# Kernel tuning notes

Measured on AMD Instinct MI355X. Metric: run time of the kernel, lower is better.

## Reference

```python
import jax, jax.numpy as jnp
import numpy as np

N = 100_000
E = 1_600_000
IN_DIM = 21
HID = 256
OUT = 256


def setup_inputs() -> dict:
    key = jax.random.key(0)
    ks = jax.random.split(key, 10)
    node_scalar = jax.random.normal(ks[0], (N, IN_DIM), dtype=jnp.float32)
    edge_index = jax.random.randint(ks[1], (2, E), 0, N, dtype=jnp.int64)
    s_in = 1.0 / np.sqrt(IN_DIM)
    s_h = 1.0 / np.sqrt(HID)
    W_in = jax.random.uniform(ks[2], (IN_DIM, HID), jnp.float32, -s_in, s_in)
    b_in = jax.random.uniform(ks[3], (HID,), jnp.float32, -s_in, s_in)
    W_self = jax.random.uniform(ks[4], (HID, HID), jnp.float32, -s_h, s_h)
    b_self = jax.random.uniform(ks[5], (HID,), jnp.float32, -s_h, s_h)
    W_nei = jax.random.uniform(ks[6], (HID, HID), jnp.float32, -s_h, s_h)
    b_nei = jax.random.uniform(ks[7], (HID,), jnp.float32, -s_h, s_h)
    W_out = jax.random.uniform(ks[8], (HID, OUT), jnp.float32, -s_h, s_h)
    b_out = jax.random.uniform(ks[9], (OUT,), jnp.float32, -s_h, s_h)
    return {
        "node_scalar": node_scalar,
        "W_in": W_in, "b_in": b_in,
        "W_self": W_self, "b_self": b_self,
        "W_nei": W_nei, "b_nei": b_nei,
        "W_out": W_out, "b_out": b_out,
        "edge_index": edge_index,
    }


def reference(node_scalar, W_in, b_in, W_self, b_self, W_nei, b_nei, W_out, b_out, edge_index):
    # x = relu(Linear(node_scalar)); dropout is identity in eval mode
    x = jax.nn.relu(node_scalar @ W_in + b_in)           # (N, H)
    n = x.shape[0]
    src, dst = edge_index[0], edge_index[1]
    msg = x[src]                                          # (E, H) gather
    agg = jax.ops.segment_sum(msg, dst, num_segments=n)   # (N, H) scatter-add
    deg = jax.ops.segment_sum(jnp.ones((dst.shape[0],), dtype=x.dtype), dst, num_segments=n)
    agg = agg / jnp.maximum(deg, 1.0)[:, None]            # degree mean (clamp_min 1)
    h = jax.nn.relu(x @ W_self + b_self + agg @ W_nei + b_nei)
    g = h.mean(axis=0)                                    # global mean pool -> (H,)
    return g @ W_out + b_out                              # (OUT,)
```

## Files before the change

### kernel.cpp

```cpp
#include <hip/hip_runtime.h>
#include <hip/hip_bf16.h>

#define HID 256
#define IND 21
#define PB 6400
#define MAXB 512

typedef short short8 __attribute__((ext_vector_type(8)));
typedef float floatx16 __attribute__((ext_vector_type(16)));
typedef float floatx2 __attribute__((ext_vector_type(2)));

__device__ inline unsigned short f2bf(float f) {
  __hip_bfloat16 h = __float2bfloat16(f);
  union { __hip_bfloat16 h; unsigned short u; } c;
  c.h = h;
  return c.u;
}

__device__ inline unsigned int pk_bf16_trunc(floatx2 p) {
  union { float f; unsigned int u; } a, b;
  a.f = p.x; b.f = p.y;
  return (b.u & 0xffff0000u) | (a.u >> 16);
}

__device__ inline void acc8p(uint2 v, floatx2* a) {
  a[0] += __builtin_amdgcn_cvt_pk_f32_fp8((int)v.x, false);
  a[1] += __builtin_amdgcn_cvt_pk_f32_fp8((int)v.x, true);
  a[2] += __builtin_amdgcn_cvt_pk_f32_fp8((int)v.y, false);
  a[3] += __builtin_amdgcn_cvt_pk_f32_fp8((int)v.y, true);
}

__device__ inline short8 mk_s8(unsigned a, unsigned b, unsigned c, unsigned d) {
  union { uint4 u; short8 s; } x; x.u = make_uint4(a, b, c, d); return x.s;
}

__device__ inline short8 dec8(uint2 v) {
  unsigned w0 = pk_bf16_trunc(__builtin_amdgcn_cvt_pk_f32_fp8((int)v.x, false));
  unsigned w1 = pk_bf16_trunc(__builtin_amdgcn_cvt_pk_f32_fp8((int)v.x, true));
  unsigned w2 = pk_bf16_trunc(__builtin_amdgcn_cvt_pk_f32_fp8((int)v.y, false));
  unsigned w3 = pk_bf16_trunc(__builtin_amdgcn_cvt_pk_f32_fp8((int)v.y, true));
  return mk_s8(w0, w1, w2, w3);
}

__device__ inline void gl16(const unsigned char* g, unsigned char* l) {
  __builtin_amdgcn_global_load_lds(
      (const __attribute__((address_space(1))) unsigned char*)g,
      (__attribute__((address_space(3))) unsigned char*)l, 16, 0, 0);
}

__global__ __launch_bounds__(256) void k_front(
    const float* __restrict__ ns, const float* __restrict__ Win,
    const float* __restrict__ bin, uint2* __restrict__ xq2,
    uint2* __restrict__ Aqx,
    const float* __restrict__ Wself, const float* __restrict__ Wnei,
    unsigned short* __restrict__ Bf16,
    const int* __restrict__ dst, int* __restrict__ bcnt,
    int N, int E, int nb2, int G1) {
  int blk = blockIdx.x;
  int tid = threadIdx.x;
  if (blk < G1) {
    __shared__ float s[8][IND];
    __shared__ float fx[8][257];
    int nb = blk * 8;
    if (tid < 8 * IND) {
      int idx = nb * IND + tid;
      s[tid / IND][tid % IND] = (idx < N * IND) ? ns[idx] : 0.f;
    }
    float w[IND];
#pragma unroll
    for (int k = 0; k < IND; k++) w[k] = Win[k * HID + tid];
    float b = bin[tid];
    __syncthreads();
#pragma unroll
    for (int j = 0; j < 8; j++) {
      float acc = b;
#pragma unroll
      for (int k = 0; k < IND; k++) acc += s[j][k] * w[k];
      fx[j][tid] = acc > 0.f ? acc : 0.f;
    }
    __syncthreads();
    {
      int j = tid & 7, u = tid >> 3;
      int node = nb + j;
      if (node < N) {
        const float* fp = &fx[j][u * 8];
        int lo0 = __builtin_amdgcn_cvt_pk_fp8_f32(fp[0], fp[1], 0, false);
        int w0  = __builtin_amdgcn_cvt_pk_fp8_f32(fp[2], fp[3], lo0, true);
        int lo1 = __builtin_amdgcn_cvt_pk_fp8_f32(fp[4], fp[5], 0, false);
        int w1  = __builtin_amdgcn_cvt_pk_fp8_f32(fp[6], fp[7], lo1, true);
        uint2 val = make_uint2((unsigned)w0, (unsigned)w1);
        xq2[(size_t)node * 32 + u] = val;
        int g = node >> 5, row = node & 31, c = u >> 1, hi = u & 1;
        Aqx[(size_t)(g * 16 + c) * 64 + hi * 32 + row] = val;
      }
    }
  } else if (blk < G1 + 256) {
    int n = blk - G1;
    int ct = n >> 5, l5 = n & 31;
#pragma unroll
    for (int t = 0; t < 2; t++) {
      int k = tid + t * 256;
      float v = (k < HID) ? Wself[k * HID + n] : Wnei[(k - HID) * HID + n];
      int c = k >> 4, kin = k & 15;
      int lane = (kin >> 3) * 32 + l5;
      int j = kin & 7;
      Bf16[(size_t)((c * 8 + ct) * 64 + lane) * 8 + j] = f2bf(v);
    }
  } else {
    __shared__ int lh[MAXB];
    int e0 = (blk - G1 - 256) * PB;
    for (int b = tid; b < nb2; b += 256) lh[b] = 0;
    __syncthreads();
    int c = min(PB, E - e0);
    for (int i = tid; i < c; i += 256) atomicAdd(&lh[dst[e0 + i] >> 8], 1);
    __syncthreads();
    for (int b = tid; b < nb2; b += 256)
      if (lh[b]) atomicAdd(&bcnt[b], lh[b]);
  }
}

__global__ __launch_bounds__(512) void k_bscan(
    const int* __restrict__ bcnt, int* __restrict__ bbase, int* __restrict__ bcur,
    int* __restrict__ row_start, int E, int N, int nb2) {
  __shared__ int ts[512];
  int tid = threadIdx.x;
  int v = (tid < nb2) ? bcnt[tid] : 0;
  ts[tid] = v;
  __syncthreads();
  for (int off = 1; off < 512; off <<= 1) {
    int t = (tid >= off) ? ts[tid - off] : 0;
    __syncthreads();
    ts[tid] += t;
    __syncthreads();
  }
  if (tid < nb2) { bbase[tid] = ts[tid] - v; bcur[tid] = ts[tid] - v; }
  if (tid == 0) { bbase[nb2] = E; row_start[N] = E; }
}

__global__ __launch_bounds__(256) void k_part(
    const int* __restrict__ src, const int* __restrict__ dst,
    int* __restrict__ bcur, unsigned int* __restrict__ ebuf, int E, int nb2) {
  __shared__ int lh[MAXB];
  int tid = threadIdx.x;
  int e0 = blockIdx.x * PB;
  for (int b = tid; b < nb2; b += 256) lh[b] = 0;
  __syncthreads();
  int cnt = min(PB, E - e0);
  for (int i = tid; i < cnt; i += 256) atomicAdd(&lh[dst[e0 + i] >> 8], 1);
  __syncthreads();
  for (int b = tid; b < nb2; b += 256) {
    int c = lh[b];
    lh[b] = (c > 0) ? atomicAdd(&bcur[b], c) : 0;
  }
  __syncthreads();
  for (int i = tid; i < cnt; i += 256) {
    int s = src[e0 + i];
    int d = dst[e0 + i];
    int pos = atomicAdd(&lh[d >> 8], 1);
    ebuf[pos] = ((unsigned)s << 8) | ((unsigned)d & 255u);
  }
}

__global__ __launch_bounds__(256) void k_fill2(
    const unsigned int* __restrict__ ebuf, const int* __restrict__ bbase,
    int* __restrict__ row_start, unsigned int* __restrict__ csr, int N) {
  __shared__ int lcnt[256];
  __shared__ int lcur[256];
  __shared__ int ts[256];
  int b = blockIdx.x;
  int tid = threadIdx.x;
  int start = bbase[b], end = bbase[b + 1];
  lcnt[tid] = 0;
  __syncthreads();
  for (int i = start + tid; i < end; i += 256)
    atomicAdd(&lcnt[ebuf[i] & 255u], 1);
  __syncthreads();
  int v = lcnt[tid];
  ts[tid] = v;
  __syncthreads();
  for (int off = 1; off < 256; off <<= 1) {
    int t = (tid >= off) ? ts[tid - off] : 0;
    __syncthreads();
    ts[tid] += t;
    __syncthreads();
  }
  int excl = start + ts[tid] - v;
  int node = (b << 8) + tid;
  if (node < N) row_start[node] = excl;
  lcur[tid] = excl;
  __syncthreads();
  for (int i = start + tid; i < end; i += 256) {
    unsigned int e = ebuf[i];
    int pos = atomicAdd(&lcur[e & 255u], 1);
    csr[pos] = e & ~255u;
  }
}

__global__ __launch_bounds__(256) void k_agg(
    const unsigned char* __restrict__ xqb, const unsigned int* __restrict__ csrb,
    const int* __restrict__ row_start, uint2* __restrict__ Aqagg, int N) {
  __shared__ uint2 ld[8][33];
  int tid = threadIdx.x;
  int lane = tid & 63;
  int w = tid >> 6;
  int half = lane >> 5;
  int l32 = lane & 31;
  unsigned lo = (unsigned)(l32 * 8);

  int nl = w * 2 + half;
  int wid = blockIdx.x * 8 + nl;
  int cw = (wid < N) ? wid : (N - 1);
  int start = row_start[cw];
  int end = row_start[cw + 1];
  int c = end - start;
  floatx2 a[4], b[4], d[4], e[4];
#pragma unroll
  for (int j = 0; j < 4; j++) {
    a[j] = (floatx2){0.f, 0.f}; b[j] = (floatx2){0.f, 0.f};
    d[j] = (floatx2){0.f, 0.f}; e[j] = (floatx2){0.f, 0.f};
  }

  int i = 0;
  while (i < c) {
    int nb = min(32, c - i);
    int sel = (l32 < nb) ? l32 : 0;
    unsigned idx = csrb[start + i + sel];
    int j = 0;
    for (; j + 8 <= nb; j += 8) {
      unsigned o0 = (unsigned)__shfl((int)idx, j + 0, 32) + lo;
      unsigned o1 = (unsigned)__shfl((int)idx, j + 1, 32) + lo;
      unsigned o2 = (unsigned)__shfl((int)idx, j + 2, 32) + lo;
      unsigned o3 = (unsigned)__shfl((int)idx, j + 3, 32) + lo;
      unsigned o4 = (unsigned)__shfl((int)idx, j + 4, 32) + lo;
      unsigned o5 = (unsigned)__shfl((int)idx, j + 5, 32) + lo;
      unsigned o6 = (unsigned)__shfl((int)idx, j + 6, 32) + lo;
      unsigned o7 = (unsigned)__shfl((int)idx, j + 7, 32) + lo;
      uint2 v0 = *(const uint2*)(xqb + o0);
      uint2 v1 = *(const uint2*)(xqb + o1);
      uint2 v2 = *(const uint2*)(xqb + o2);
      uint2 v3 = *(const uint2*)(xqb + o3);
      uint2 v4 = *(const uint2*)(xqb + o4);
      uint2 v5 = *(const uint2*)(xqb + o5);
      uint2 v6 = *(const uint2*)(xqb + o6);
      uint2 v7 = *(const uint2*)(xqb + o7);
      acc8p(v0, a); acc8p(v1, b); acc8p(v2, d); acc8p(v3, e);
      acc8p(v4, a); acc8p(v5, b); acc8p(v6, d); acc8p(v7, e);
    }
    for (; j + 4 <= nb; j += 4) {
      unsigned o0 = (unsigned)__shfl((int)idx, j + 0, 32) + lo;
      unsigned o1 = (unsigned)__shfl((int)idx, j + 1, 32) + lo;
      unsigned o2 = (unsigned)__shfl((int)idx, j + 2, 32) + lo;
      unsigned o3 = (unsigned)__shfl((int)idx, j + 3, 32) + lo;
      uint2 v0 = *(const uint2*)(xqb + o0);
      uint2 v1 = *(const uint2*)(xqb + o1);
      uint2 v2 = *(const uint2*)(xqb + o2);
      uint2 v3 = *(const uint2*)(xqb + o3);
      acc8p(v0, a); acc8p(v1, b); acc8p(v2, d); acc8p(v3, e);
    }
    for (; j < nb; j++) {
      unsigned o0 = (unsigned)__shfl((int)idx, j, 32) + lo;
      uint2 v0 = *(const uint2*)(xqb + o0);
      acc8p(v0, a);
    }
    i += nb;
  }
#pragma unroll
  for (int j = 0; j < 4; j++) a[j] += b[j] + d[j] + e[j];

  float inv = 1.0f / fmaxf((float)c, 1.0f);
  float f[8];
#pragma unroll
  for (int j = 0; j < 4; j++) {
    f[2 * j] = a[j].x * inv;
    f[2 * j + 1] = a[j].y * inv;
  }
  int lo0 = __builtin_amdgcn_cvt_pk_fp8_f32(f[0], f[1], 0, false);
  int w0  = __builtin_amdgcn_cvt_pk_fp8_f32(f[2], f[3], lo0, true);
  int lo1 = __builtin_amdgcn_cvt_pk_fp8_f32(f[4], f[5], 0, false);
  int w1  = __builtin_amdgcn_cvt_pk_fp8_f32(f[6], f[7], lo1, true);
  ld[nl][l32] = make_uint2((unsigned)w0, (unsigned)w1);
  __syncthreads();

  int g = blockIdx.x >> 2;
  int r0 = (blockIdx.x & 3) * 8;
  int s = tid >> 3, j = tid & 7;
  Aqagg[(size_t)g * 1024 + (size_t)s * 32 + r0 + j] = ld[j][s];
}

__global__ __launch_bounds__(256, 3) void k_h(
    const unsigned char* __restrict__ Aqx, const unsigned char* __restrict__ Aqagg,
    const unsigned char* __restrict__ Bf8, const float* __restrict__ bself,
    const float* __restrict__ bnei, float* __restrict__ hpart, int N, int nfull) {
  __shared__ __align__(16) unsigned char As[2][8192];
  __shared__ __align__(16) unsigned char Bs[2][16384];
  __shared__ float colsum[128];
  int bid = blockIdx.x;
  int bx, by;
  if (bid < nfull) {
    bx = (bid >> 4) * 8 + (bid & 7);
    by = (bid >> 3) & 1;
  } else {
    int rem = bid - nfull;
    bx = (nfull >> 1) + (rem >> 1);
    by = rem & 1;
  }
  int tid = threadIdx.x;
  int lane = tid & 63;
  int w = tid >> 6;
  int wr = w >> 1, wc = w & 1;
  int l32 = lane & 31, half = lane >> 5;
  int rowBase = bx * 128;

  if (tid < 128) colsum[tid] = 0.f;

  floatx16 acc[2][2];
#pragma unroll
  for (int i = 0; i < 2; i++)
#pragma unroll
    for (int j = 0; j < 2; j++) acc[i][j] = (floatx16)(0.f);

  size_t a_grp = (size_t)(bx * 4 + w) * 16 * 512;
  int lb = lane * 16;

  {
    const unsigned char* asrc = Aqx + a_grp + lb;
    gl16(asrc, As[0] + w * 2048);
    gl16(asrc + 1024, As[0] + w * 2048 + 1024);
#pragma unroll
    for (int fi = 0; fi < 4; fi++) {
      int ctg = by * 4 + fi;
      gl16(Bf8 + (size_t)(w * 8 + ctg) * 1024 + lb, Bs[0] + (w * 4 + fi) * 1024);
    }
  }

  for (int ch = 0; ch < 8; ch++) {
    int buf = ch & 1;
    __syncthreads();
    if (ch < 7) {
      int cn = ch + 1;
      const unsigned char* Aq = (cn < 4) ? Aqx : Aqagg;
      const unsigned char* asrc = Aq + a_grp + (size_t)(cn & 3) * 2048 + lb;
      unsigned char* ad = As[buf ^ 1] + w * 2048;
      gl16(asrc, ad);
      gl16(asrc + 1024, ad + 1024);
#pragma unroll
      for (int fi = 0; fi < 4; fi++) {
        int cg = cn * 4 + w;
        int ctg = by * 4 + fi;
        gl16(Bf8 + (size_t)(cg * 8 + ctg) * 1024 + lb,
             Bs[buf ^ 1] + (w * 4 + fi) * 1024);
      }
    }
#pragma unroll
    for (int cl = 0; cl < 4; cl++) {
      short8 afr[2];
#pragma unroll
      for (int rt = 0; rt < 2; rt++) {
        uint2 av = *(const uint2*)&As[buf][(wr * 2 + rt) * 2048 + cl * 512 + lane * 8];
        afr[rt] = dec8(av);
      }
#pragma unroll
      for (int ctw = 0; ctw < 2; ctw++) {
        short8 bfr = *(const short8*)&Bs[buf][(cl * 4 + wc * 2 + ctw) * 1024 + lane * 16];
#pragma unroll
        for (int rt = 0; rt < 2; rt++)
          acc[rt][ctw] = __builtin_amdgcn_mfma_f32_32x32x16_bf16(
              afr[rt], bfr, acc[rt][ctw], 0, 0, 0);
      }
    }
  }

#pragma unroll
  for (int ctw = 0; ctw < 2; ctw++) {
    int lcol = (wc * 2 + ctw) * 32 + l32;
    int gcol = by * 128 + lcol;
    float bb = bself[gcol] + bnei[gcol];
    float psum = 0.f;
#pragma unroll
    for (int rt = 0; rt < 2; rt++) {
#pragma unroll
      for (int r = 0; r < 16; r++) {
        int rw = rowBase + wr * 64 + rt * 32 + (r & 3) + 8 * (r >> 2) + 4 * half;
        float v = acc[rt][ctw][r] + bb;
        v = v > 0.f ? v : 0.f;
        if (rw < N) psum += v;
      }
    }
    atomicAdd(&colsum[lcol], psum);
  }
  __syncthreads();
  if (tid < 128) hpart[(size_t)bx * 256 + by * 128 + tid] = colsum[tid];
}

__global__ __launch_bounds__(256) void k_red(
    const float* __restrict__ hpart, float* __restrict__ gsum, int nbx) {
  int c = threadIdx.x;
  float s = 0.f;
  for (int i = blockIdx.x; i < nbx; i += gridDim.x)
    s += hpart[(size_t)i * 256 + c];
  atomicAdd(&gsum[c], s);
}

__global__ __launch_bounds__(HID) void k_out(
    const float* __restrict__ gsum, const float* __restrict__ Wout,
    const float* __restrict__ bout, float* __restrict__ out, float invN) {
  __shared__ float g[HID];
  int c = threadIdx.x;
  g[c] = gsum[c] * invN;
  __syncthreads();
  float acc = bout[c];
#pragma unroll 8
  for (int k = 0; k < HID; k++) acc += g[k] * Wout[k * HID + c];
  out[c] = acc;
}

extern "C" void kernel_launch(void* const* d_in, const int* in_sizes, int n_in,
                              void* d_out, int out_size, void* d_ws, size_t ws_size,
                              hipStream_t stream) {
  const float* ns    = (const float*)d_in[0];
  const float* Win   = (const float*)d_in[1];
  const float* bin   = (const float*)d_in[2];
  const float* Wself = (const float*)d_in[3];
  const float* bself = (const float*)d_in[4];
  const float* Wnei  = (const float*)d_in[5];
  const float* bnei  = (const float*)d_in[6];
  const float* Wout  = (const float*)d_in[7];
  const float* bout  = (const float*)d_in[8];
  const int*   eidx  = (const int*)d_in[9];

  int N = in_sizes[0] / IND;
  int E = in_sizes[9] / 2;
  const int* src = eidx;
  const int* dst = eidx + E;
  int nb2 = (N + 255) >> 8;
  int nbx = (N + 127) / 128;
  size_t NGU = (size_t)nbx * 4 * 16 * 64;

  unsigned int* xq     = (unsigned int*)d_ws;
  uint2* Aqx           = (uint2*)(xq + (size_t)N * 64);
  uint2* Aqagg         = Aqx + NGU;
  unsigned short* Bf16 = (unsigned short*)(Aqagg + NGU);
  unsigned int* csr  = (unsigned int*)(Bf16 + 256 * 512);
  unsigned int* ebuf = csr + E;
  int* row_start = (int*)(ebuf + E);
  int* bcnt      = row_start + N + 1;
  int* bbase     = bcnt + MAXB;
  int* bcur      = bbase + MAXB + 1;
  float* gsum    = (float*)(bcur + MAXB);
  float* hpart   = gsum + HID;

  hipMemsetAsync(bcnt, 0, MAXB * sizeof(int), stream);
  hipMemsetAsync(gsum, 0, HID * sizeof(float), stream);

  int G1 = (N + 7) / 8;
  int pgrid = (E + PB - 1) / PB;
  k_front<<<G1 + 256 + pgrid, 256, 0, stream>>>(
      ns, Win, bin, (uint2*)xq, Aqx, Wself, Wnei, Bf16, dst, bcnt,
      N, E, nb2, G1);

  k_bscan<<<1, 512, 0, stream>>>(bcnt, bbase, bcur, row_start, E, N, nb2);
  k_part<<<pgrid, 256, 0, stream>>>(src, dst, bcur, ebuf, E, nb2);
  k_fill2<<<nb2, 256, 0, stream>>>(ebuf, bbase, row_start, csr, N);

  int agrid = (N + 7) / 8;
  k_agg<<<agrid, 256, 0, stream>>>((const unsigned char*)xq, csr, row_start,
                                   Aqagg, N);

  int nblocks = nbx * 2;
  int nfull = (nblocks / 16) * 16;
  k_h<<<nblocks, 256, 0, stream>>>((const unsigned char*)Aqx,
                                   (const unsigned char*)Aqagg,
                                   (const unsigned char*)Bf16,
                                   bself, bnei, hpart, N, nfull);

  k_red<<<64, 256, 0, stream>>>(hpart, gsum, nbx);
  k_out<<<1, HID, 0, stream>>>(gsum, Wout, bout, (float*)d_out, 1.0f / (float)N);
}
```

Before: 284.1 us.

## Fuse neighbor aggregation into the GEMM kernel and drop hpart reduction

```diff
diff --git a/kernel.cpp b/kernel.cpp
--- a/kernel.cpp
+++ b/kernel.cpp
@@ -196,122 +196,110 @@
   }
 }
 
-__global__ __launch_bounds__(256) void k_agg(
+__global__ __launch_bounds__(256, 3) void k_hagg(
     const unsigned char* __restrict__ xqb, const unsigned int* __restrict__ csrb,
-    const int* __restrict__ row_start, uint2* __restrict__ Aqagg, int N) {
-  __shared__ uint2 ld[8][33];
+    const int* __restrict__ row_start, const unsigned char* __restrict__ Aqx,
+    const unsigned short* __restrict__ Bf16, const float* __restrict__ bself,
+    const float* __restrict__ bnei, float* __restrict__ gsum, int N) {
+  __shared__ __align__(16) unsigned char As[2][4096];
+  __shared__ __align__(16) unsigned char AggL[16384];
+  __shared__ float colsum[256];
   int tid = threadIdx.x;
   int lane = tid & 63;
   int w = tid >> 6;
-  int half = lane >> 5;
-  int l32 = lane & 31;
-  unsigned lo = (unsigned)(l32 * 8);
-
-  int nl = w * 2 + half;
-  int wid = blockIdx.x * 8 + nl;
-  int cw = (wid < N) ? wid : (N - 1);
-  int start = row_start[cw];
-  int end = row_start[cw + 1];
-  int c = end - start;
-  floatx2 a[4], b[4], d[4], e[4];
-#pragma unroll
-  for (int j = 0; j < 4; j++) {
-    a[j] = (floatx2){0.f, 0.f}; b[j] = (floatx2){0.f, 0.f};
-    d[j] = (floatx2){0.f, 0.f}; e[j] = (floatx2){0.f, 0.f};
-  }
-
-  int i = 0;
-  while (i < c) {
-    int nb = min(32, c - i);
-    int sel = (l32 < nb) ? l32 : 0;
-    unsigned idx = csrb[start + i + sel];
-    int j = 0;
-    for (; j + 8 <= nb; j += 8) {
-      unsigned o0 = (unsigned)__shfl((int)idx, j + 0, 32) + lo;
-      unsigned o1 = (unsigned)__shfl((int)idx, j + 1, 32) + lo;
-      unsigned o2 = (unsigned)__shfl((int)idx, j + 2, 32) + lo;
-      unsigned o3 = (unsigned)__shfl((int)idx, j + 3, 32) + lo;
-      unsigned o4 = (unsigned)__shfl((int)idx, j + 4, 32) + lo;
-      unsigned o5 = (unsigned)__shfl((int)idx, j + 5, 32) + lo;
-      unsigned o6 = (unsigned)__shfl((int)idx, j + 6, 32) + lo;
-      unsigned o7 = (unsigned)__shfl((int)idx, j + 7, 32) + lo;
-      uint2 v0 = *(const uint2*)(xqb + o0);
-      uint2 v1 = *(const uint2*)(xqb + o1);
-      uint2 v2 = *(const uint2*)(xqb + o2);
-      uint2 v3 = *(const uint2*)(xqb + o3);
-      uint2 v4 = *(const uint2*)(xqb + o4);
-      uint2 v5 = *(const uint2*)(xqb + o5);
-      uint2 v6 = *(const uint2*)(xqb + o6);
-      uint2 v7 = *(const uint2*)(xqb + o7);
-      acc8p(v0, a); acc8p(v1, b); acc8p(v2, d); acc8p(v3, e);
-      acc8p(v4, a); acc8p(v5, b); acc8p(v6, d); acc8p(v7, e);
-    }
-    for (; j + 4 <= nb; j += 4) {
-      unsigned o0 = (unsigned)__shfl((int)idx, j + 0, 32) + lo;
-      unsigned o1 = (unsigned)__shfl((int)idx, j + 1, 32) + lo;
-      unsigned o2 = (unsigned)__shfl((int)idx, j + 2, 32) + lo;
-      unsigned o3 = (unsigned)__shfl((int)idx, j + 3, 32) + lo;
-      uint2 v0 = *(const uint2*)(xqb + o0);
-      uint2 v1 = *(const uint2*)(xqb + o1);
-      uint2 v2 = *(const uint2*)(xqb + o2);
-      uint2 v3 = *(const uint2*)(xqb + o3);
-      acc8p(v0, a); acc8p(v1, b); acc8p(v2, d); acc8p(v3, e);
-    }
-    for (; j < nb; j++) {
-      unsigned o0 = (unsigned)__shfl((int)idx, j, 32) + lo;
-      uint2 v0 = *(const uint2*)(xqb + o0);
-      acc8p(v0, a);
-    }
-    i += nb;
-  }
-#pragma unroll
-  for (int j = 0; j < 4; j++) a[j] += b[j] + d[j] + e[j];
-
-  float inv = 1.0f / fmaxf((float)c, 1.0f);
-  float f[8];
-#pragma unroll
-  for (int j = 0; j < 4; j++) {
-    f[2 * j] = a[j].x * inv;
-    f[2 * j + 1] = a[j].y * inv;
-  }
-  int lo0 = __builtin_amdgcn_cvt_pk_fp8_f32(f[0], f[1], 0, false);
-  int w0  = __builtin_amdgcn_cvt_pk_fp8_f32(f[2], f[3], lo0, true);
-  int lo1 = __builtin_amdgcn_cvt_pk_fp8_f32(f[4], f[5], 0, false);
-  int w1  = __builtin_amdgcn_cvt_pk_fp8_f32(f[6], f[7], lo1, true);
-  ld[nl][l32] = make_uint2((unsigned)w0, (unsigned)w1);
-  __syncthreads();
-
-  int g = blockIdx.x >> 2;
-  int r0 = (blockIdx.x & 3) * 8;
-  int s = tid >> 3, j = tid & 7;
-  Aqagg[(size_t)g * 1024 + (size_t)s * 32 + r0 + j] = ld[j][s];
-}
-
-__global__ __launch_bounds__(256, 3) void k_h(
-    const unsigned char* __restrict__ Aqx, const unsigned char* __restrict__ Aqagg,
-    const unsigned char* __restrict__ Bf8, const float* __restrict__ bself,
-    const float* __restrict__ bnei, float* __restrict__ hpart, int N, int nfull) {
-  __shared__ __align__(16) unsigned char As[2][8192];
-  __shared__ __align__(16) unsigned char Bs[2][16384];
-  __shared__ float colsum[128];
-  int bid = blockIdx.x;
-  int bx, by;
-  if (bid < nfull) {
-    bx = (bid >> 4) * 8 + (bid & 7);
-    by = (bid >> 3) & 1;
-  } else {
-    int rem = bid - nfull;
-    bx = (nfull >> 1) + (rem >> 1);
-    by = rem & 1;
-  }
-  int tid = threadIdx.x;
-  int lane = tid & 63;
-  int w = tid >> 6;
-  int wr = w >> 1, wc = w & 1;
+  int bx = blockIdx.x;
+  int rowBase = bx * 64;
   int l32 = lane & 31, half = lane >> 5;
-  int rowBase = bx * 128;
-
-  if (tid < 128) colsum[tid] = 0.f;
+
+  colsum[tid] = 0.f;
+
+  int gi = w >> 1, kb = w & 1;
+  {
+    const unsigned char* asrc =
+        Aqx + (size_t)(bx * 2 + gi) * 8192 + kb * 1024 + lane * 16;
+    gl16(asrc, As[0] + gi * 2048 + kb * 1024);
+  }
+
+  {
+    unsigned lo = (unsigned)(l32 * 8);
+    unsigned u = (unsigned)l32;
+    unsigned ubase = (u >> 3) * 512 + ((u & 7) >> 1) * 64 + (u & 1) * 32;
+    uint2* AggL2 = (uint2*)AggL;
+    for (int pass = 0; pass < 8; ++pass) {
+      int nd = pass * 8 + w * 2 + half;
+      int wid = rowBase + nd;
+      int cw = (wid < N) ? wid : (N - 1);
+      int start = row_start[cw];
+      int end = row_start[cw + 1];
+      int c = end - start;
+      floatx2 a[4], b[4];
+#pragma unroll
+      for (int j = 0; j < 4; j++) {
+        a[j] = (floatx2){0.f, 0.f};
+        b[j] = (floatx2){0.f, 0.f};
+      }
+      int i = 0;
+      while (i < c) {
+        int nb = min(32, c - i);
+        int sel = (l32 < nb) ? l32 : 0;
+        unsigned idx = csrb[start + i + sel];
+        int j = 0;
+        for (; j + 8 <= nb; j += 8) {
+          unsigned o0 = (unsigned)__shfl((int)idx, j + 0, 32) + lo;
+          unsigned o1 = (unsigned)__shfl((int)idx, j + 1, 32) + lo;
+          unsigned o2 = (unsigned)__shfl((int)idx, j + 2, 32) + lo;
+          unsigned o3 = (unsigned)__shfl((int)idx, j + 3, 32) + lo;
+          unsigned o4 = (unsigned)__shfl((int)idx, j + 4, 32) + lo;
+          unsigned o5 = (unsigned)__shfl((int)idx, j + 5, 32) + lo;
+          unsigned o6 = (unsigned)__shfl((int)idx, j + 6, 32) + lo;
+          unsigned o7 = (unsigned)__shfl((int)idx, j + 7, 32) + lo;
+          uint2 v0 = *(const uint2*)(xqb + o0);
+          uint2 v1 = *(const uint2*)(xqb + o1);
+          uint2 v2 = *(const uint2*)(xqb + o2);
+          uint2 v3 = *(const uint2*)(xqb + o3);
+          uint2 v4 = *(const uint2*)(xqb + o4);
+          uint2 v5 = *(const uint2*)(xqb + o5);
+          uint2 v6 = *(const uint2*)(xqb + o6);
+          uint2 v7 = *(const uint2*)(xqb + o7);
+          acc8p(v0, a); acc8p(v1, b); acc8p(v2, a); acc8p(v3, b);
+          acc8p(v4, a); acc8p(v5, b); acc8p(v6, a); acc8p(v7, b);
+        }
+        for (; j + 4 <= nb; j += 4) {
+          unsigned o0 = (unsigned)__shfl((int)idx, j + 0, 32) + lo;
+          unsigned o1 = (unsigned)__shfl((int)idx, j + 1, 32) + lo;
+          unsigned o2 = (unsigned)__shfl((int)idx, j + 2, 32) + lo;
+          unsigned o3 = (unsigned)__shfl((int)idx, j + 3, 32) + lo;
+          uint2 v0 = *(const uint2*)(xqb + o0);
+          uint2 v1 = *(const uint2*)(xqb + o1);
+          uint2 v2 = *(const uint2*)(xqb + o2);
+          uint2 v3 = *(const uint2*)(xqb + o3);
+          acc8p(v0, a); acc8p(v1, b); acc8p(v2, a); acc8p(v3, b);
+        }
+        for (; j < nb; j++) {
+          unsigned o0 = (unsigned)__shfl((int)idx, j, 32) + lo;
+          uint2 v0 = *(const uint2*)(xqb + o0);
+          acc8p(v0, a);
+        }
+        i += nb;
+      }
+#pragma unroll
+      for (int j = 0; j < 4; j++) a[j] += b[j];
+
+      float inv = 1.0f / fmaxf((float)c, 1.0f);
+      float f[8];
+#pragma unroll
+      for (int j = 0; j < 4; j++) {
+        f[2 * j] = a[j].x * inv;
+        f[2 * j + 1] = a[j].y * inv;
+      }
+      int lo0 = __builtin_amdgcn_cvt_pk_fp8_f32(f[0], f[1], 0, false);
+      int w0  = __builtin_amdgcn_cvt_pk_fp8_f32(f[2], f[3], lo0, true);
+      int lo1 = __builtin_amdgcn_cvt_pk_fp8_f32(f[4], f[5], 0, false);
+      int w1  = __builtin_amdgcn_cvt_pk_fp8_f32(f[6], f[7], lo1, true);
+      AggL2[ubase + (unsigned)((nd >> 5) * 256 + (nd & 31))] =
+          make_uint2((unsigned)w0, (unsigned)w1);
+    }
+  }
 
   floatx16 acc[2][2];
 #pragma unroll
@@ -319,86 +307,74 @@
 #pragma unroll
     for (int j = 0; j < 2; j++) acc[i][j] = (floatx16)(0.f);
 
-  size_t a_grp = (size_t)(bx * 4 + w) * 16 * 512;
-  int lb = lane * 16;
-
-  {
-    const unsigned char* asrc = Aqx + a_grp + lb;
-    gl16(asrc, As[0] + w * 2048);
-    gl16(asrc + 1024, As[0] + w * 2048 + 1024);
-#pragma unroll
-    for (int fi = 0; fi < 4; fi++) {
-      int ctg = by * 4 + fi;
-      gl16(Bf8 + (size_t)(w * 8 + ctg) * 1024 + lb, Bs[0] + (w * 4 + fi) * 1024);
-    }
-  }
-
-  for (int ch = 0; ch < 8; ch++) {
-    int buf = ch & 1;
-    __syncthreads();
-    if (ch < 7) {
-      int cn = ch + 1;
-      const unsigned char* Aq = (cn < 4) ? Aqx : Aqagg;
-      const unsigned char* asrc = Aq + a_grp + (size_t)(cn & 3) * 2048 + lb;
-      unsigned char* ad = As[buf ^ 1] + w * 2048;
-      gl16(asrc, ad);
-      gl16(asrc + 1024, ad + 1024);
-#pragma unroll
-      for (int fi = 0; fi < 4; fi++) {
-        int cg = cn * 4 + w;
-        int ctg = by * 4 + fi;
-        gl16(Bf8 + (size_t)(cg * 8 + ctg) * 1024 + lb,
-             Bs[buf ^ 1] + (w * 4 + fi) * 1024);
-      }
-    }
-#pragma unroll
-    for (int cl = 0; cl < 4; cl++) {
+  int buf = 0;
+  for (int ch = 0; ch < 4; ++ch) {
+    __syncthreads();
+    if (ch < 3) {
+      const unsigned char* asrc = Aqx + (size_t)(bx * 2 + gi) * 8192 +
+                                  (size_t)(ch + 1) * 2048 + kb * 1024 + lane * 16;
+      gl16(asrc, As[buf ^ 1] + gi * 2048 + kb * 1024);
+    }
+#pragma unroll
+    for (int cl = 0; cl < 4; ++cl) {
       short8 afr[2];
 #pragma unroll
-      for (int rt = 0; rt < 2; rt++) {
-        uint2 av = *(const uint2*)&As[buf][(wr * 2 + rt) * 2048 + cl * 512 + lane * 8];
-        afr[rt] = dec8(av);
-      }
-#pragma unroll
-      for (int ctw = 0; ctw < 2; ctw++) {
-        short8 bfr = *(const short8*)&Bs[buf][(cl * 4 + wc * 2 + ctw) * 1024 + lane * 16];
-#pragma unroll
-        for (int rt = 0; rt < 2; rt++)
+      for (int rt = 0; rt < 2; ++rt)
+        afr[rt] = dec8(*(const uint2*)&As[buf][rt * 2048 + cl * 512 + lane * 8]);
+      int cfull = ch * 4 + cl;
+#pragma unroll
+      for (int ctw = 0; ctw < 2; ++ctw) {
+        int ct = w * 2 + ctw;
+        short8 bfr = *(const short8*)&Bf16[((size_t)(cfull * 8 + ct) * 64 + lane) * 8];
+#pragma unroll
+        for (int rt = 0; rt < 2; ++rt)
           acc[rt][ctw] = __builtin_amdgcn_mfma_f32_32x32x16_bf16(
               afr[rt], bfr, acc[rt][ctw], 0, 0, 0);
       }
     }
-  }
-
-#pragma unroll
-  for (int ctw = 0; ctw < 2; ctw++) {
-    int lcol = (wc * 2 + ctw) * 32 + l32;
-    int gcol = by * 128 + lcol;
+    buf ^= 1;
+  }
+#pragma unroll
+  for (int ch = 4; ch < 8; ++ch) {
+    const unsigned char* Ab = AggL + (size_t)(ch - 4) * 4096;
+#pragma unroll
+    for (int cl = 0; cl < 4; ++cl) {
+      short8 afr[2];
+#pragma unroll
+      for (int rt = 0; rt < 2; ++rt)
+        afr[rt] = dec8(*(const uint2*)&Ab[rt * 2048 + cl * 512 + lane * 8]);
+      int cfull = ch * 4 + cl;
+#pragma unroll
+      for (int ctw = 0; ctw < 2; ++ctw) {
+        int ct = w * 2 + ctw;
+        short8 bfr = *(const short8*)&Bf16[((size_t)(cfull * 8 + ct) * 64 + lane) * 8];
+#pragma unroll
+        for (int rt = 0; rt < 2; ++rt)
+          acc[rt][ctw] = __builtin_amdgcn_mfma_f32_32x32x16_bf16(
+              afr[rt], bfr, acc[rt][ctw], 0, 0, 0);
+      }
+    }
+  }
+
+#pragma unroll
+  for (int ctw = 0; ctw < 2; ++ctw) {
+    int gcol = (w * 2 + ctw) * 32 + l32;
     float bb = bself[gcol] + bnei[gcol];
     float psum = 0.f;
 #pragma unroll
-    for (int rt = 0; rt < 2; rt++) {
-#pragma unroll
-      for (int r = 0; r < 16; r++) {
-        int rw = rowBase + wr * 64 + rt * 32 + (r & 3) + 8 * (r >> 2) + 4 * half;
+    for (int rt = 0; rt < 2; ++rt) {
+#pragma unroll
+      for (int r = 0; r < 16; ++r) {
+        int rw = rowBase + rt * 32 + (r & 3) + 8 * (r >> 2) + 4 * half;
         float v = acc[rt][ctw][r] + bb;
         v = v > 0.f ? v : 0.f;
         if (rw < N) psum += v;
       }
     }
-    atomicAdd(&colsum[lcol], psum);
-  }
-  __syncthreads();
-  if (tid < 128) hpart[(size_t)bx * 256 + by * 128 + tid] = colsum[tid];
-}
-
-__global__ __launch_bounds__(256) void k_red(
-    const float* __restrict__ hpart, float* __restrict__ gsum, int nbx) {
-  int c = threadIdx.x;
-  float s = 0.f;
-  for (int i = blockIdx.x; i < nbx; i += gridDim.x)
-    s += hpart[(size_t)i * 256 + c];
-  atomicAdd(&gsum[c], s);
+    atomicAdd(&colsum[gcol], psum);
+  }
+  __syncthreads();
+  atomicAdd(&gsum[tid], colsum[tid]);
 }
 
 __global__ __launch_bounds__(HID) void k_out(
@@ -447,7 +423,6 @@
   int* bbase     = bcnt + MAXB;
   int* bcur      = bbase + MAXB + 1;
   float* gsum    = (float*)(bcur + MAXB);
-  float* hpart   = gsum + HID;
 
   hipMemsetAsync(bcnt, 0, MAXB * sizeof(int), stream);
   hipMemsetAsync(gsum, 0, HID * sizeof(float), stream);
@@ -462,17 +437,11 @@
   k_part<<<pgrid, 256, 0, stream>>>(src, dst, bcur, ebuf, E, nb2);
   k_fill2<<<nb2, 256, 0, stream>>>(ebuf, bbase, row_start, csr, N);
 
-  int agrid = (N + 7) / 8;
-  k_agg<<<agrid, 256, 0, stream>>>((const unsigned char*)xq, csr, row_start,
-                                   Aqagg, N);
-
-  int nblocks = nbx * 2;
-  int nfull = (nblocks / 16) * 16;
-  k_h<<<nblocks, 256, 0, stream>>>((const unsigned char*)Aqx,
-                                   (const unsigned char*)Aqagg,
-                                   (const unsigned char*)Bf16,
-                                   bself, bnei, hpart, N, nfull);
-
-  k_red<<<64, 256, 0, stream>>>(hpart, gsum, nbx);
+  int hgrid = (N + 63) / 64;
+  k_hagg<<<hgrid, 256, 0, stream>>>((const unsigned char*)xq, csr, row_start,
+                                    (const unsigned char*)Aqx,
+                                    (const unsigned short*)Bf16,
+                                    bself, bnei, gsum, N);
+
   k_out<<<1, HID, 0, stream>>>(gsum, Wout, bout, (float*)d_out, 1.0f / (float)N);
 }
```

After: 294.5 us. 1.04x slower.

## Build CSR via per-node degree atomics and direct scatter instead of bucket partition

Applied to the files above, without the earlier changes.

```diff
diff --git a/kernel.cpp b/kernel.cpp
--- a/kernel.cpp
+++ b/kernel.cpp
@@ -54,8 +54,8 @@
     uint2* __restrict__ Aqx,
     const float* __restrict__ Wself, const float* __restrict__ Wnei,
     unsigned short* __restrict__ Bf16,
-    const int* __restrict__ dst, int* __restrict__ bcnt,
-    int N, int E, int nb2, int G1) {
+    const int* __restrict__ dst, int* __restrict__ deg,
+    int N, int E, int G1) {
   int blk = blockIdx.x;
   int tid = threadIdx.x;
   if (blk < G1) {
@@ -107,24 +107,37 @@
       Bf16[(size_t)((c * 8 + ct) * 64 + lane) * 8 + j] = f2bf(v);
     }
   } else {
-    __shared__ int lh[MAXB];
     int e0 = (blk - G1 - 256) * PB;
-    for (int b = tid; b < nb2; b += 256) lh[b] = 0;
-    __syncthreads();
     int c = min(PB, E - e0);
-    for (int i = tid; i < c; i += 256) atomicAdd(&lh[dst[e0 + i] >> 8], 1);
-    __syncthreads();
-    for (int b = tid; b < nb2; b += 256)
-      if (lh[b]) atomicAdd(&bcnt[b], lh[b]);
-  }
+    for (int i = tid; i < c; i += 256) atomicAdd(&deg[dst[e0 + i]], 1);
+  }
+}
+
+__global__ __launch_bounds__(256) void k_scan1(
+    const int* __restrict__ deg, int* __restrict__ lpre,
+    int* __restrict__ bsum, int N) {
+  __shared__ int ts[256];
+  int tid = threadIdx.x;
+  int n = blockIdx.x * 256 + tid;
+  int v = (n < N) ? deg[n] : 0;
+  ts[tid] = v;
+  __syncthreads();
+  for (int off = 1; off < 256; off <<= 1) {
+    int t = (tid >= off) ? ts[tid - off] : 0;
+    __syncthreads();
+    ts[tid] += t;
+    __syncthreads();
+  }
+  if (n < N) lpre[n] = ts[tid] - v;
+  if (tid == 255) bsum[blockIdx.x] = ts[255];
 }
 
 __global__ __launch_bounds__(512) void k_bscan(
-    const int* __restrict__ bcnt, int* __restrict__ bbase, int* __restrict__ bcur,
+    const int* __restrict__ bsum, int* __restrict__ bbase,
     int* __restrict__ row_start, int E, int N, int nb2) {
   __shared__ int ts[512];
   int tid = threadIdx.x;
-  int v = (tid < nb2) ? bcnt[tid] : 0;
+  int v = (tid < nb2) ? bsum[tid] : 0;
   ts[tid] = v;
   __syncthreads();
   for (int off = 1; off < 512; off <<= 1) {
@@ -133,66 +146,31 @@
     ts[tid] += t;
     __syncthreads();
   }
-  if (tid < nb2) { bbase[tid] = ts[tid] - v; bcur[tid] = ts[tid] - v; }
-  if (tid == 0) { bbase[nb2] = E; row_start[N] = E; }
-}
-
-__global__ __launch_bounds__(256) void k_part(
+  if (tid < nb2) bbase[tid] = ts[tid] - v;
+  if (tid == 0) row_start[N] = E;
+}
+
+__global__ __launch_bounds__(256) void k_scan2(
+    const int* __restrict__ lpre, const int* __restrict__ bbase,
+    int* __restrict__ row_start, int* __restrict__ cursor, int N) {
+  int n = blockIdx.x * 256 + threadIdx.x;
+  if (n < N) {
+    int rs = bbase[n >> 8] + lpre[n];
+    row_start[n] = rs;
+    cursor[n] = rs;
+  }
+}
+
+__global__ __launch_bounds__(256) void k_scatter(
     const int* __restrict__ src, const int* __restrict__ dst,
-    int* __restrict__ bcur, unsigned int* __restrict__ ebuf, int E, int nb2) {
-  __shared__ int lh[MAXB];
-  int tid = threadIdx.x;
+    int* __restrict__ cursor, unsigned int* __restrict__ csr, int E) {
   int e0 = blockIdx.x * PB;
-  for (int b = tid; b < nb2; b += 256) lh[b] = 0;
-  __syncthreads();
-  int cnt = min(PB, E - e0);
-  for (int i = tid; i < cnt; i += 256) atomicAdd(&lh[dst[e0 + i] >> 8], 1);
-  __syncthreads();
-  for (int b = tid; b < nb2; b += 256) {
-    int c = lh[b];
-    lh[b] = (c > 0) ? atomicAdd(&bcur[b], c) : 0;
-  }
-  __syncthreads();
-  for (int i = tid; i < cnt; i += 256) {
+  int c = min(PB, E - e0);
+  for (int i = threadIdx.x; i < c; i += 256) {
     int s = src[e0 + i];
     int d = dst[e0 + i];
-    int pos = atomicAdd(&lh[d >> 8], 1);
-    ebuf[pos] = ((unsigned)s << 8) | ((unsigned)d & 255u);
-  }
-}
-
-__global__ __launch_bounds__(256) void k_fill2(
-    const unsigned int* __restrict__ ebuf, const int* __restrict__ bbase,
-    int* __restrict__ row_start, unsigned int* __restrict__ csr, int N) {
-  __shared__ int lcnt[256];
-  __shared__ int lcur[256];
-  __shared__ int ts[256];
-  int b = blockIdx.x;
-  int tid = threadIdx.x;
-  int start = bbase[b], end = bbase[b + 1];
-  lcnt[tid] = 0;
-  __syncthreads();
-  for (int i = start + tid; i < end; i += 256)
-    atomicAdd(&lcnt[ebuf[i] & 255u], 1);
-  __syncthreads();
-  int v = lcnt[tid];
-  ts[tid] = v;
-  __syncthreads();
-  for (int off = 1; off < 256; off <<= 1) {
-    int t = (tid >= off) ? ts[tid - off] : 0;
-    __syncthreads();
-    ts[tid] += t;
-    __syncthreads();
-  }
-  int excl = start + ts[tid] - v;
-  int node = (b << 8) + tid;
-  if (node < N) row_start[node] = excl;
-  lcur[tid] = excl;
-  __syncthreads();
-  for (int i = start + tid; i < end; i += 256) {
-    unsigned int e = ebuf[i];
-    int pos = atomicAdd(&lcur[e & 255u], 1);
-    csr[pos] = e & ~255u;
+    int pos = atomicAdd(&cursor[d], 1);
+    csr[pos] = (unsigned)s << 8;
   }
 }
 
@@ -219,7 +197,6 @@
     a[j] = (floatx2){0.f, 0.f}; b[j] = (floatx2){0.f, 0.f};
     d[j] = (floatx2){0.f, 0.f}; e[j] = (floatx2){0.f, 0.f};
   }
-
   int i = 0;
   while (i < c) {
     int nb = min(32, c - i);
@@ -441,26 +418,27 @@
   uint2* Aqagg         = Aqx + NGU;
   unsigned short* Bf16 = (unsigned short*)(Aqagg + NGU);
   unsigned int* csr  = (unsigned int*)(Bf16 + 256 * 512);
-  unsigned int* ebuf = csr + E;
-  int* row_start = (int*)(ebuf + E);
-  int* bcnt      = row_start + N + 1;
-  int* bbase     = bcnt + MAXB;
-  int* bcur      = bbase + MAXB + 1;
-  float* gsum    = (float*)(bcur + MAXB);
+  int* deg       = (int*)(csr + E);
+  int* lpre      = deg + N;
+  int* cursor    = lpre + N;
+  int* bsum      = cursor + N;
+  int* row_start = bsum + MAXB;
+  int* bbase     = row_start + N + 1;
+  float* gsum    = (float*)(bbase + MAXB + 1);
   float* hpart   = gsum + HID;
 
-  hipMemsetAsync(bcnt, 0, MAXB * sizeof(int), stream);
+  hipMemsetAsync(deg, 0, (size_t)N * sizeof(int), stream);
   hipMemsetAsync(gsum, 0, HID * sizeof(float), stream);
 
   int G1 = (N + 7) / 8;
   int pgrid = (E + PB - 1) / PB;
   k_front<<<G1 + 256 + pgrid, 256, 0, stream>>>(
-      ns, Win, bin, (uint2*)xq, Aqx, Wself, Wnei, Bf16, dst, bcnt,
-      N, E, nb2, G1);
-
-  k_bscan<<<1, 512, 0, stream>>>(bcnt, bbase, bcur, row_start, E, N, nb2);
-  k_part<<<pgrid, 256, 0, stream>>>(src, dst, bcur, ebuf, E, nb2);
-  k_fill2<<<nb2, 256, 0, stream>>>(ebuf, bbase, row_start, csr, N);
+      ns, Win, bin, (uint2*)xq, Aqx, Wself, Wnei, Bf16, dst, deg, N, E, G1);
+
+  k_scan1<<<nb2, 256, 0, stream>>>(deg, lpre, bsum, N);
+  k_bscan<<<1, 512, 0, stream>>>(bsum, bbase, row_start, E, N, nb2);
+  k_scan2<<<(N + 255) / 256, 256, 0, stream>>>(lpre, bbase, row_start, cursor, N);
+  k_scatter<<<pgrid, 256, 0, stream>>>(src, dst, cursor, csr, E);
 
   int agrid = (N + 7) / 8;
   k_agg<<<agrid, 256, 0, stream>>>((const unsigned char*)xq, csr, row_start,
```

After: 427.7 us. 50.6% more time.
